# Optimization experiments

Hardware: AMD Instinct MI355X
Metric: run time of the kernel (lower is better)

The kernel has to match this reference:

```python
import jax, jax.numpy as jnp
import numpy as np
from jax import lax

# ---- static config (matches init_kwargs) ----
STRIDE = 16
BASE_SIZE = 16
SCALES = np.array([2., 4., 8., 16., 32.])
RATIOS = np.array([0.5, 1., 2.])
CLIP = 4.14
NMS_THRESH = 0.7
PRE_NMS = 6000
POST_NMS = 300
MIN_SIZE = 16.0


def _whctrs(a):
    w = a[2] - a[0] + 1.0
    h = a[3] - a[1] + 1.0
    return w, h, a[0] + 0.5 * (w - 1.0), a[1] + 0.5 * (h - 1.0)


def _mkanchors(ws, hs, xc, yc):
    return np.stack([xc - 0.5 * (ws - 1.0), yc - 0.5 * (hs - 1.0),
                     xc + 0.5 * (ws - 1.0), yc + 0.5 * (hs - 1.0)], axis=1)


def _base_anchors():
    ba = np.array([1.0, 1.0, BASE_SIZE, BASE_SIZE]) - 1.0
    w, h, xc, yc = _whctrs(ba)
    size = w * h
    ws = np.round(np.sqrt(size / RATIOS))
    hs = np.round(ws * RATIOS)
    ra = _mkanchors(ws, hs, xc, yc)
    out = []
    for i in range(ra.shape[0]):
        w, h, xc, yc = _whctrs(ra[i])
        out.append(_mkanchors(w * SCALES, h * SCALES, xc, yc))
    return np.concatenate(out, axis=0)  # (A,4), A = len(ratios)*len(scales)


def _grid_anchors(Hf, Wf):
    ba = _base_anchors()                       # (A,4)
    sx, sy = np.meshgrid(np.arange(Wf) * STRIDE, np.arange(Hf) * STRIDE)
    shifts = np.stack([sx, sy, sx, sy], axis=-1)          # (Hf,Wf,4)
    anch = shifts[:, :, None, :] + ba[None, None, :, :]    # (Hf,Wf,A,4)
    return jnp.asarray(anch.reshape(1, -1, 4), dtype=jnp.float32)


def _decode_clip(anchors, deltas, img_h, img_w):
    # NormalizedBoxCenterDecoder (stds=1) + clip to image
    aw = anchors[..., 2] - anchors[..., 0]
    ah = anchors[..., 3] - anchors[..., 1]
    ax = anchors[..., 0] + 0.5 * aw
    ay = anchors[..., 1] + 0.5 * ah
    dx, dy, dw, dh = deltas[..., 0], deltas[..., 1], deltas[..., 2], deltas[..., 3]
    ox = dx * aw + ax
    oy = dy * ah + ay
    ow = jnp.exp(jnp.minimum(dw, CLIP)) * aw * 0.5
    oh = jnp.exp(jnp.minimum(dh, CLIP)) * ah * 0.5
    x1 = jnp.clip(ox - ow, 0.0, img_w - 1.0)
    y1 = jnp.clip(oy - oh, 0.0, img_h - 1.0)
    x2 = jnp.clip(ox + ow, 0.0, img_w - 1.0)
    y2 = jnp.clip(oy + oh, 0.0, img_h - 1.0)
    return jnp.stack([x1, y1, x2, y2], axis=-1)


def _nms_single(scores, boxes):
    # scores (N,), boxes (N,4). Greedy NMS, force_suppress, sorted by score desc.
    order = jnp.argsort(-scores)[:PRE_NMS]
    s = scores[order]
    b = boxes[order]
    x1, y1, x2, y2 = b[:, 0], b[:, 1], b[:, 2], b[:, 3]
    area = (x2 - x1) * (y2 - y1)
    iw = jnp.maximum(jnp.minimum(x2[:, None], x2[None, :]) - jnp.maximum(x1[:, None], x1[None, :]), 0.0)
    ih = jnp.maximum(jnp.minimum(y2[:, None], y2[None, :]) - jnp.maximum(y1[:, None], y1[None, :]), 0.0)
    inter = iw * ih
    iou = inter / (area[:, None] + area[None, :] - inter + 1e-12)  # (PRE,PRE)

    supp0 = s < 0.0  # invalid entries (score set to -1 by min_size filter)

    def body(supp, i):
        keep = jnp.logical_not(supp[i])
        new = jnp.where(keep, jnp.logical_or(supp, iou[i] > NMS_THRESH), supp)
        new = new.at[i].set(supp[i])  # never self-suppress
        return new, None

    supp, _ = lax.scan(body, supp0, jnp.arange(PRE_NMS))
    kept = jnp.logical_not(supp)
    perm = jnp.argsort(jnp.where(kept, 0, 1), stable=True)  # kept boxes first, order preserved
    out_s = jnp.where(kept[perm], s[perm], -1.0)
    out_b = jnp.where(kept[perm][:, None], b[perm], -1.0)
    return out_s[:POST_NMS, None], out_b[:POST_NMS]


def _forward(img, x, conv_w, conv_b, score_w, score_b, loc_w, loc_b):
    B, _, Hf, Wf = x.shape
    img_h, img_w = float(img.shape[2]), float(img.shape[3])
    anchors = _grid_anchors(Hf, Wf)  # (1, Hf*Wf*A, 4)

    # conv1 3x3 pad 1 + ReLU
    h = lax.conv_general_dilated(x, conv_w, (1, 1), [(1, 1), (1, 1)],
                                 dimension_numbers=('NCHW', 'OIHW', 'NCHW'))
    h = jax.nn.relu(h + conv_b[None, :, None, None])

    A = score_w.shape[0]
    raw_scores = jnp.einsum('bchw,oc->bhwo', h, score_w.reshape(A, -1)) + score_b
    raw_scores = raw_scores.reshape(B, -1, 1)                       # (B,N,1)
    raw_boxes = jnp.einsum('bchw,oc->bhwo', h, loc_w.reshape(4 * A, -1)) + loc_b
    raw_boxes = raw_boxes.reshape(B, -1, 4)                         # (B,N,4)

    rpn_scores = jax.nn.sigmoid(raw_scores)

    roi = _decode_clip(anchors, raw_boxes, img_h, img_w)            # (B,N,4)
    width = roi[..., 2] - roi[..., 0]
    height = roi[..., 3] - roi[..., 1]
    invalid = jnp.logical_or(width < MIN_SIZE, height < MIN_SIZE)   # (B,N)
    score = jnp.where(invalid[..., None], -1.0, rpn_scores)         # (B,N,1)
    roi = jnp.where(invalid[..., None], -1.0, roi)

    out_s, out_b = jax.vmap(_nms_single)(score[..., 0], roi)        # (B,300,1),(B,300,4)
    return jnp.concatenate([out_s, out_b], axis=-1)                 # (B,300,5)


def setup_inputs() -> dict:
    key = jax.random.key(0)
    ks = jax.random.split(key, 8)
    img = jax.random.normal(ks[0], (1, 3, 1024, 1024), jnp.float32)
    x = jax.random.normal(ks[1], (1, 1024, 64, 64), jnp.float32)
    conv_w = jax.random.normal(ks[2], (1024, 1024, 3, 3), jnp.float32) * 0.01
    conv_b = jnp.zeros((1024,), jnp.float32)
    score_w = jax.random.normal(ks[3], (15, 1024, 1, 1), jnp.float32) * 0.01
    score_b = jnp.zeros((15,), jnp.float32)
    loc_w = jax.random.normal(ks[4], (60, 1024, 1, 1), jnp.float32) * 0.002
    loc_b = jnp.zeros((60,), jnp.float32)
    return {"img": img, "x": x, "conv_w": conv_w, "conv_b": conv_b,
            "score_w": score_w, "score_b": score_b, "loc_w": loc_w, "loc_b": loc_b}


def reference(img, x, conv_w, conv_b, score_w, score_b, loc_w, loc_b):
    return _forward(img, x, conv_w, conv_b, score_w, score_b, loc_w, loc_b)
```

## Files before the change

### kernel.cpp

```cpp
#include <hip/hip_runtime.h>

typedef unsigned int uint;
typedef unsigned short ushort;
typedef unsigned long long u64;

typedef __attribute__((ext_vector_type(8))) short short8;
typedef __attribute__((ext_vector_type(4))) float floatx4;

__device__ inline ushort bf16rne(float v) {
  uint b = __float_as_uint(v);
  uint r = (b + 0x7fffu + ((b >> 16) & 1u)) >> 16;
  return (ushort)r;
}

__device__ inline void gl_lds16(const void* g, void* l) {
  __builtin_amdgcn_global_load_lds(
      (const __attribute__((address_space(1))) unsigned int*)g,
      (__attribute__((address_space(3))) unsigned int*)l, 16, 0, 0);
}

__global__ __launch_bounds__(256) void prep_x(const float* __restrict__ x,
                                              ushort* __restrict__ xh,
                                              ushort* __restrict__ xl) {
  __shared__ float tile[64 * 65];
  int ci0 = blockIdx.x * 64, y = blockIdx.y, t = threadIdx.x;
#pragma unroll
  for (int it = 0; it < 16; ++it) {
    int L = t + 256 * it;
    int cl = L >> 6, xx = L & 63;
    tile[cl * 65 + xx] = x[(size_t)(ci0 + cl) * 4096 + y * 64 + xx];
  }
  __syncthreads();
#pragma unroll
  for (int it = 0; it < 16; ++it) {
    int L = t + 256 * it;
    int xx = L >> 6, cl = L & 63;
    float v = tile[cl * 65 + xx];
    ushort h2 = bf16rne(v);
    float hf = __uint_as_float((uint)h2 << 16);
    ushort l2 = bf16rne(v - hf);
    size_t oi = ((size_t)((y + 1) * 66 + (xx + 1))) * 1024 + ci0 + cl;
    xh[oi] = h2;
    xl[oi] = l2;
  }
}

__global__ __launch_bounds__(256) void prep_w(const float* __restrict__ w,
                                              ushort* __restrict__ wh,
                                              ushort* __restrict__ wl) {
  __shared__ float tile[2304];
  int co = blockIdx.x, ci0 = blockIdx.y * 256, t = threadIdx.x;
  const float* src = w + ((size_t)co * 1024 + ci0) * 9;
  for (int i = t; i < 2304; i += 256) tile[i] = src[i];
  __syncthreads();
  int ci = ci0 + t;
#pragma unroll
  for (int off = 0; off < 9; ++off) {
    float v = tile[t * 9 + off];
    ushort h2 = bf16rne(v);
    float hf = __uint_as_float((uint)h2 << 16);
    ushort l2 = bf16rne(v - hf);
    size_t oi = ((size_t)off << 20) | ((size_t)co << 10) | (size_t)ci;
    wh[oi] = h2;
    wl[oi] = l2;
  }
}

__global__ __launch_bounds__(256) void prep_head(
    const float* __restrict__ score_w, const float* __restrict__ loc_w,
    const float* __restrict__ score_b, const float* __restrict__ loc_b,
    ushort* __restrict__ wh, ushort* __restrict__ wl, float* __restrict__ bh) {
  int idx = blockIdx.x * 256 + threadIdx.x;
  int o = idx >> 10, ci = idx & 1023;
  float v = 0.f;
  if (o < 15) v = score_w[o * 1024 + ci];
  else if (o < 75) v = loc_w[(o - 15) * 1024 + ci];
  ushort h2 = bf16rne(v);
  float hf = __uint_as_float((uint)h2 << 16);
  wh[idx] = h2;
  wl[idx] = bf16rne(v - hf);
  if (idx < 128) bh[idx] = (idx < 15) ? score_b[idx] : ((idx < 75) ? loc_b[idx - 15] : 0.f);
}

template <int IM2COL>
__global__ __launch_bounds__(256, 1) void gemm_bf16x3(
    const ushort* __restrict__ Ahi, const ushort* __restrict__ Alo,
    const ushort* __restrict__ Bhi, const ushort* __restrict__ Blo,
    const float* __restrict__ bias, int nChunks, float* __restrict__ outRaw,
    ushort* __restrict__ outHi, ushort* __restrict__ outLo) {
  __shared__ ushort sm[2 * 4 * 128 * 32];
  const int t = threadIdx.x;
  const int m0 = blockIdx.x * 128;
  const int n0 = blockIdx.y * 128;

  auto stage = [&](int kc, int bufIdx) {
    char* lds = (char*)sm + bufIdx * 32768;
    int off = 0, cc = 0, oy = 0, ox = 0;
    if (IM2COL) {
      off = kc >> 5;
      cc = (kc & 31) << 5;
      oy = off / 3;
      ox = off - 3 * oy;
    }
#pragma unroll
    for (int q = 0; q < 2; ++q) {
      int L = t + 256 * q, row = L >> 2, seg = L & 3;
      size_t aoff, boff;
      if (IM2COL) {
        int m = m0 + row, y = m >> 6, xq = m & 63;
        aoff = ((size_t)((y + oy) * 66 + (xq + ox)) * 1024 + (size_t)cc) * 2 + seg * 16;
        boff = (((size_t)off << 20) + ((size_t)(n0 + row) << 10) + (size_t)cc) * 2 + seg * 16;
      } else {
        aoff = (((size_t)(m0 + row) << 10) + (size_t)kc * 32) * 2 + seg * 16;
        boff = (((size_t)(n0 + row) << 10) + (size_t)kc * 32) * 2 + seg * 16;
      }
      int dst = L * 16;
      gl_lds16((const char*)Ahi + aoff, lds + dst);
      gl_lds16((const char*)Alo + aoff, lds + 8192 + dst);
      gl_lds16((const char*)Bhi + boff, lds + 16384 + dst);
      gl_lds16((const char*)Blo + boff, lds + 24576 + dst);
    }
  };

  const int lane = t & 63, wv = t >> 6;
  const int wm = (wv & 1) * 64, wn = (wv >> 1) * 64;
  const int arow = wm + (lane & 15);
  const int brow = wn + (lane & 15);
  const int ko = (lane >> 4) * 8;

  floatx4 acc[4][4];
#pragma unroll
  for (int i = 0; i < 4; ++i)
#pragma unroll
    for (int j = 0; j < 4; ++j) acc[i][j] = (floatx4){0.f, 0.f, 0.f, 0.f};

  stage(0, 0);
  for (int kc = 0; kc < nChunks; ++kc) {
    __syncthreads();
    if (kc + 1 < nChunks) stage(kc + 1, (kc + 1) & 1);
    const ushort* sb = sm + (kc & 1) * 16384;
    const ushort* sAh = sb;
    const ushort* sAl = sb + 4096;
    const ushort* sBh = sb + 8192;
    const ushort* sBl = sb + 12288;
    short8 ah[4], al[4], bh2[4], bl2[4];
#pragma unroll
    for (int i = 0; i < 4; ++i) {
      ah[i] = *(const short8*)(sAh + (arow + 16 * i) * 32 + ko);
      al[i] = *(const short8*)(sAl + (arow + 16 * i) * 32 + ko);
      bh2[i] = *(const short8*)(sBh + (brow + 16 * i) * 32 + ko);
      bl2[i] = *(const short8*)(sBl + (brow + 16 * i) * 32 + ko);
    }
#pragma unroll
    for (int i = 0; i < 4; ++i)
#pragma unroll
      for (int j = 0; j < 4; ++j) {
        acc[i][j] = __builtin_amdgcn_mfma_f32_16x16x32_bf16(ah[i], bh2[j], acc[i][j], 0, 0, 0);
        acc[i][j] = __builtin_amdgcn_mfma_f32_16x16x32_bf16(ah[i], bl2[j], acc[i][j], 0, 0, 0);
        acc[i][j] = __builtin_amdgcn_mfma_f32_16x16x32_bf16(al[i], bh2[j], acc[i][j], 0, 0, 0);
      }
  }

#pragma unroll
  for (int i = 0; i < 4; ++i)
#pragma unroll
    for (int j = 0; j < 4; ++j) {
      int nn = n0 + wn + 16 * j + (lane & 15);
      float bv = bias[nn];
#pragma unroll
      for (int r = 0; r < 4; ++r) {
        int mm = m0 + wm + 16 * i + (lane >> 4) * 4 + r;
        float v = acc[i][j][r] + bv;
        if (IM2COL) {
          v = fmaxf(v, 0.f);
          ushort h2 = bf16rne(v);
          float hf = __uint_as_float((uint)h2 << 16);
          ushort l2 = bf16rne(v - hf);
          outHi[(size_t)mm * 1024 + nn] = h2;
          outLo[(size_t)mm * 1024 + nn] = l2;
        } else {
          outRaw[(size_t)mm * 128 + nn] = v;
        }
      }
    }
}

__global__ __launch_bounds__(256) void decode_k(const float* __restrict__ raw,
                                                float* __restrict__ scores,
                                                float4* __restrict__ boxes,
                                                uint* __restrict__ key32,
                                                uint* __restrict__ hist) {
  int i = blockIdx.x * 256 + threadIdx.x;
  int m = i / 15, a = i - m * 15;
  int y = m >> 6, x = m & 63;
  const float* rp = raw + (size_t)m * 128;
  float logit = rp[a];
  float dx = rp[15 + 4 * a], dy = rp[16 + 4 * a];
  float dw = rp[17 + 4 * a], dh = rp[18 + 4 * a];
  int rr = a / 5, ss = a - rr * 5;
  float sc5 = (float)(2 << ss);
  float W = ((rr == 0) ? 23.f : (rr == 1) ? 16.f : 11.f) * sc5;
  float H = ((rr == 0) ? 12.f : (rr == 1) ? 16.f : 22.f) * sc5;
  float aw = W - 1.f, ah = H - 1.f;
  float ax = x * 16.f + 7.5f, ay = y * 16.f + 7.5f;
  float ox = dx * aw + ax, oyc = dy * ah + ay;
  float ow = expf(fminf(dw, 4.14f)) * aw * 0.5f;
  float oh = expf(fminf(dh, 4.14f)) * ah * 0.5f;
  float x1 = fminf(fmaxf(ox - ow, 0.f), 1023.f);
  float y1 = fminf(fmaxf(oyc - oh, 0.f), 1023.f);
  float x2 = fminf(fmaxf(ox + ow, 0.f), 1023.f);
  float y2 = fminf(fmaxf(oyc + oh, 0.f), 1023.f);
  bool inval = ((x2 - x1) < 16.f) || ((y2 - y1) < 16.f);
  float sc = inval ? -1.f : (1.f / (1.f + expf(-logit)));
  scores[i] = sc;
  boxes[i] = inval ? make_float4(-1.f, -1.f, -1.f, -1.f) : make_float4(x1, y1, x2, y2);
  uint kb = __float_as_uint(sc);
  uint key = (kb & 0x80000000u) ? ~kb : (kb | 0x80000000u);
  key32[i] = key;
  atomicAdd(&hist[key >> 16], 1u);
}

__global__ __launch_bounds__(256) void find_t16(const uint* __restrict__ hist,
                                                uint* __restrict__ selT) {
  __shared__ uint ps[256];
  __shared__ int segS;
  int t = threadIdx.x;
  uint s = 0;
  const uint* hp = hist + t * 256;
  for (int i = 0; i < 256; ++i) s += hp[i];
  ps[t] = s;
  __syncthreads();
  for (int d = 1; d < 256; d <<= 1) {
    uint v = ps[t] + ((t + d < 256) ? ps[t + d] : 0u);
    __syncthreads();
    ps[t] = v;
    __syncthreads();
  }
  if (ps[t] >= 6000u && (t == 255 || ps[t + 1] < 6000u)) segS = t;
  __syncthreads();
  int sg = segS;
  uint base = (sg == 255) ? 0u : ps[sg + 1];
  uint h2 = hist[sg * 256 + t];
  __syncthreads();
  ps[t] = h2;
  __syncthreads();
  for (int d = 1; d < 256; d <<= 1) {
    uint v = ps[t] + ((t + d < 256) ? ps[t + d] : 0u);
    __syncthreads();
    ps[t] = v;
    __syncthreads();
  }
  if (base + ps[t] >= 6000u && (t == 255 || base + ps[t + 1] < 6000u))
    *selT = (uint)(sg * 256 + t);
}

__global__ __launch_bounds__(256) void gather_k(const uint* __restrict__ key32,
                                                const uint* __restrict__ selT,
                                                uint* __restrict__ cnt,
                                                u64* __restrict__ cand) {
  int i = blockIdx.x * 256 + threadIdx.x;
  uint T = *selT;
  uint k = key32[i];
  if ((k >> 16) >= T) {
    uint pos = atomicAdd(cnt, 1u);
    if (pos < 8192) cand[pos] = ((u64)k << 32) | (u64)(~(uint)i);
  }
}

__global__ __launch_bounds__(1024) void sort_gather(
    const u64* __restrict__ cand, const uint* __restrict__ cnt,
    const float* __restrict__ scores, const float4* __restrict__ boxes,
    float* __restrict__ sortedS, float4* __restrict__ sortedB) {
  extern __shared__ u64 sk[];
  int t = threadIdx.x;
  int C = (int)*cnt;
  if (C > 8192) C = 8192;
  for (int j = t; j < 8192; j += 1024) sk[j] = (j < C) ? cand[j] : 0ull;
  __syncthreads();
  for (int k = 2; k <= 8192; k <<= 1) {
    for (int j2 = k >> 1; j2 > 0; j2 >>= 1) {
      for (int p = t; p < 4096; p += 1024) {
        int i = ((p & ~(j2 - 1)) << 1) | (p & (j2 - 1));
        int ix = i | j2;
        u64 a = sk[i], b = sk[ix];
        bool ddir = (i & k) != 0;
        if ((a < b) != ddir) { sk[i] = b; sk[ix] = a; }
      }
      __syncthreads();
    }
  }
  for (int j = t; j < 6016; j += 1024) {
    if (j < 6000) {
      u64 key = sk[j];
      uint idx = ~(uint)(key & 0xffffffffu);
      sortedS[j] = scores[idx];
      sortedB[j] = boxes[idx];
    } else {
      sortedS[j] = -1.f;
      sortedB[j] = make_float4(0.f, 0.f, 0.f, 0.f);
    }
  }
}

__global__ __launch_bounds__(64) void iou_mask(const float4* __restrict__ boxes,
                                               u64* __restrict__ mask) {
  __shared__ float cx1[64], cy1[64], cx2[64], cy2[64], car[64];
  int bi = blockIdx.x, bj = blockIdx.y, t = threadIdx.x;
  float4 cb = boxes[bj * 64 + t];
  cx1[t] = cb.x; cy1[t] = cb.y; cx2[t] = cb.z; cy2[t] = cb.w;
  car[t] = (cb.z - cb.x) * (cb.w - cb.y);
  __syncthreads();
  int r = bi * 64 + t;
  float4 rb = boxes[r];
  float ra = (rb.z - rb.x) * (rb.w - rb.y);
  u64 wd = 0;
#pragma unroll 8
  for (int j = 0; j < 64; ++j) {
    float iw = fmaxf(fminf(rb.z, cx2[j]) - fmaxf(rb.x, cx1[j]), 0.f);
    float ih = fmaxf(fminf(rb.w, cy2[j]) - fmaxf(rb.y, cy1[j]), 0.f);
    float inter = iw * ih;
    float iou = inter / (ra + car[j] - inter + 1e-12f);
    if (iou > 0.7f && r != bj * 64 + j) wd |= (1ull << j);
  }
  mask[(size_t)r * 128 + bj] = wd;
}

__global__ __launch_bounds__(64) void nms_scan(const u64* __restrict__ mask,
                                               const float* __restrict__ sortedS,
                                               const float4* __restrict__ sortedB,
                                               float* __restrict__ out) {
  __shared__ int klist[300];
  int lane = threadIdx.x;
  u64 Sx = 0, Sy = 0;
  for (int w2 = 0; w2 < 94; ++w2) {
    bool neg = sortedS[w2 * 64 + lane] < 0.f;
    u64 m2 = __ballot(neg);
    if ((w2 >> 1) == lane) { if (w2 & 1) Sy = m2; else Sx = m2; }
  }
  int count = 0;
  for (int w2 = 0; w2 < 94; ++w2) {
    u64 cur = __shfl((w2 & 1) ? Sy : Sx, w2 >> 1);
    u64 rem = ~cur;
    if (w2 == 93) rem &= (1ull << 48) - 1;
    while (rem) {
      int b = __builtin_ctzll(rem);
      int i = w2 * 64 + b;
      if (lane == 0) klist[count] = i;
      count++;
      if (count == 300) goto done;
      const ulonglong2* rp = (const ulonglong2*)(mask + (size_t)i * 128);
      ulonglong2 rv = rp[lane];
      Sx |= rv.x;
      Sy |= rv.y;
      u64 cur2 = __shfl((w2 & 1) ? Sy : Sx, w2 >> 1);
      rem &= ~cur2;
      rem &= (b == 63) ? 0ull : (~0ull << (b + 1));
    }
  }
done:
  __syncthreads();
  for (int j = lane; j < 300; j += 64) {
    float s;
    float4 bb;
    if (j < count) {
      int i = klist[j];
      s = sortedS[i];
      bb = sortedB[i];
    } else {
      s = -1.f;
      bb = make_float4(-1.f, -1.f, -1.f, -1.f);
    }
    out[j * 5 + 0] = s;
    out[j * 5 + 1] = bb.x;
    out[j * 5 + 2] = bb.y;
    out[j * 5 + 3] = bb.z;
    out[j * 5 + 4] = bb.w;
  }
}

constexpr size_t O_XH = 0;
constexpr size_t O_XL = 8921088;
constexpr size_t O_WTH = 17842176;
constexpr size_t O_WTL = 36716544;
constexpr size_t O_HH = 55590912;
constexpr size_t O_HL = 63979520;
constexpr size_t O_WHH = 72368128;
constexpr size_t O_WHL = 72630272;
constexpr size_t O_BHD = 72892416;
constexpr size_t O_SC = 72892928;
constexpr size_t O_BX = 73138688;
constexpr size_t O_KEY = 74121728;
constexpr size_t O_HIST = 74367488;
constexpr size_t O_CNT = 74629632;
constexpr size_t O_CAND = 74629888;
constexpr size_t O_SELT = 74695424;
constexpr size_t O_SS = 74695680;
constexpr size_t O_SB = 74719744;
constexpr size_t O_RAW = 0;
constexpr size_t O_MASK = 17842176;

extern "C" void kernel_launch(void* const* d_in, const int* in_sizes, int n_in,
                              void* d_out, int out_size, void* d_ws,
                              size_t ws_size, hipStream_t stream) {
  (void)in_sizes; (void)n_in; (void)out_size; (void)ws_size;
  const float* x = (const float*)d_in[1];
  const float* conv_w = (const float*)d_in[2];
  const float* conv_b = (const float*)d_in[3];
  const float* score_w = (const float*)d_in[4];
  const float* score_b = (const float*)d_in[5];
  const float* loc_w = (const float*)d_in[6];
  const float* loc_b = (const float*)d_in[7];
  float* out = (float*)d_out;
  char* ws = (char*)d_ws;

  ushort* xh = (ushort*)(ws + O_XH);
  ushort* xl = (ushort*)(ws + O_XL);
  ushort* wTh = (ushort*)(ws + O_WTH);
  ushort* wTl = (ushort*)(ws + O_WTL);
  ushort* hh = (ushort*)(ws + O_HH);
  ushort* hl = (ushort*)(ws + O_HL);
  ushort* wHh = (ushort*)(ws + O_WHH);
  ushort* wHl = (ushort*)(ws + O_WHL);
  float* biasH = (float*)(ws + O_BHD);
  float* raw = (float*)(ws + O_RAW);
  float* scores = (float*)(ws + O_SC);
  float4* boxes = (float4*)(ws + O_BX);
  uint* key32 = (uint*)(ws + O_KEY);
  uint* hist = (uint*)(ws + O_HIST);
  uint* cnt = (uint*)(ws + O_CNT);
  u64* cand = (u64*)(ws + O_CAND);
  uint* selT = (uint*)(ws + O_SELT);
  float* sortedS = (float*)(ws + O_SS);
  float4* sortedB = (float4*)(ws + O_SB);
  u64* mask = (u64*)(ws + O_MASK);

  hipMemsetAsync(ws + O_XH, 0, 2 * 8921088, stream);
  hipMemsetAsync(ws + O_HIST, 0, 262144 + 256, stream);

  prep_x<<<dim3(16, 64), 256, 0, stream>>>(x, xh, xl);
  prep_w<<<dim3(1024, 4), 256, 0, stream>>>(conv_w, wTh, wTl);
  prep_head<<<512, 256, 0, stream>>>(score_w, loc_w, score_b, loc_b, wHh, wHl, biasH);

  gemm_bf16x3<1><<<dim3(32, 8), 256, 0, stream>>>(xh, xl, wTh, wTl, conv_b, 288,
                                                  nullptr, hh, hl);
  gemm_bf16x3<0><<<dim3(32, 1), 256, 0, stream>>>(hh, hl, wHh, wHl, biasH, 32,
                                                  raw, nullptr, nullptr);

  decode_k<<<240, 256, 0, stream>>>(raw, scores, boxes, key32, hist);
  find_t16<<<1, 256, 0, stream>>>(hist, selT);
  gather_k<<<240, 256, 0, stream>>>(key32, selT, cnt, cand);
  sort_gather<<<1, 1024, 65536, stream>>>(cand, cnt, scores, boxes, sortedS, sortedB);
  iou_mask<<<dim3(94, 94), 64, 0, stream>>>(sortedB, mask);
  nms_scan<<<1, 64, 0, stream>>>(mask, sortedS, sortedB, out);
}
```

Before: 743.9 us.

## Replace single-block bitonic sort with histogram bucket scatter and per-bucket sorts

Replaces the single-workgroup 8192-element bitonic sort of the top-k candidates with an exclusive scan over the 65536-bin score histogram. Candidates are scattered directly into their bucket positions, then each small bucket is sorted in parallel by its own workgroup. The NMS scan also prefetches the next candidate's mask row so its load overlaps the current iteration. This removes a long serial-ish sort in one block but adds extra kernel launches, a memset, and atomics per bucket.

```diff
diff --git a/kernel.cpp b/kernel.cpp
--- a/kernel.cpp
+++ b/kernel.cpp
@@ -220,85 +220,100 @@
   atomicAdd(&hist[key >> 16], 1u);
 }
 
-__global__ __launch_bounds__(256) void find_t16(const uint* __restrict__ hist,
-                                                uint* __restrict__ selT) {
-  __shared__ uint ps[256];
-  __shared__ int segS;
+__global__ __launch_bounds__(1024) void scan_hist(const uint* __restrict__ hist,
+                                                  uint* __restrict__ bbase,
+                                                  uint* __restrict__ selC) {
+  __shared__ uint cs[1024];
   int t = threadIdx.x;
+  const uint* hp = hist + t * 64;
   uint s = 0;
-  const uint* hp = hist + t * 256;
-  for (int i = 0; i < 256; ++i) s += hp[i];
-  ps[t] = s;
+#pragma unroll 8
+  for (int i = 0; i < 64; ++i) s += hp[i];
+  cs[t] = s;
   __syncthreads();
-  for (int d = 1; d < 256; d <<= 1) {
-    uint v = ps[t] + ((t + d < 256) ? ps[t + d] : 0u);
+  for (int d = 1; d < 1024; d <<= 1) {
+    uint v = cs[t] + ((t + d < 1024) ? cs[t + d] : 0u);
     __syncthreads();
-    ps[t] = v;
+    cs[t] = v;
     __syncthreads();
   }
-  if (ps[t] >= 6000u && (t == 255 || ps[t + 1] < 6000u)) segS = t;
-  __syncthreads();
-  int sg = segS;
-  uint base = (sg == 255) ? 0u : ps[sg + 1];
-  uint h2 = hist[sg * 256 + t];
-  __syncthreads();
-  ps[t] = h2;
-  __syncthreads();
-  for (int d = 1; d < 256; d <<= 1) {
-    uint v = ps[t] + ((t + d < 256) ? ps[t + d] : 0u);
+  uint above = (t < 1023) ? cs[t + 1] : 0u;
+  uint run = 0;
+  for (int i = 63; i >= 0; --i) {
+    uint h = hp[i];
+    uint ca = above + run;
+    bbase[t * 64 + i] = ca;
+    if (ca < 6000u && ca + h >= 6000u) {
+      selC[0] = (uint)(t * 64 + i);
+      selC[1] = ca + h;
+    }
+    run += h;
+  }
+}
+
+__global__ __launch_bounds__(256) void scatter_k(const uint* __restrict__ key32,
+                                                 const uint* __restrict__ bbase,
+                                                 const uint* __restrict__ selC,
+                                                 uint* __restrict__ fill,
+                                                 u64* __restrict__ sby) {
+  int i = blockIdx.x * 256 + threadIdx.x;
+  uint k = key32[i];
+  uint b = k >> 16;
+  if (b >= selC[0]) {
+    uint pos = bbase[b] + atomicAdd(&fill[b], 1u);
+    if (pos < 8192) sby[pos] = ((u64)k << 32) | (u64)(~(uint)i);
+  }
+}
+
+__global__ __launch_bounds__(64) void bucket_sort(const uint* __restrict__ bbase,
+                                                  const uint* __restrict__ selC,
+                                                  u64* __restrict__ sby) {
+  __shared__ u64 sk[4096];
+  uint T = selC[0], C = selC[1];
+  int lane = threadIdx.x;
+  for (uint b = T + blockIdx.x; b < 65536u; b += 8192u) {
+    uint base = bbase[b];
+    if (base >= 6000u) continue;
+    uint incl = (b == 0) ? C : bbase[b - 1];
+    uint n = incl - base;
+    if (n < 2u || n > 4096u) continue;
+    if (base + n > 8192u) continue;
+    uint np2 = 1;
+    while (np2 < n) np2 <<= 1;
+    for (uint j = lane; j < np2; j += 64) sk[j] = (j < n) ? sby[base + j] : 0ull;
     __syncthreads();
-    ps[t] = v;
+    for (uint k = 2; k <= np2; k <<= 1) {
+      for (uint j2 = k >> 1; j2 > 0; j2 >>= 1) {
+        for (uint p = lane; p < (np2 >> 1); p += 64) {
+          uint i1 = ((p & ~(j2 - 1)) << 1) | (p & (j2 - 1));
+          uint ix = i1 | j2;
+          u64 a = sk[i1], c = sk[ix];
+          bool descseg = (i1 & k) == 0;
+          if ((a < c) == descseg) { sk[i1] = c; sk[ix] = a; }
+        }
+        __syncthreads();
+      }
+    }
+    for (uint j = lane; j < n; j += 64) sby[base + j] = sk[j];
     __syncthreads();
   }
-  if (base + ps[t] >= 6000u && (t == 255 || base + ps[t + 1] < 6000u))
-    *selT = (uint)(sg * 256 + t);
-}
-
-__global__ __launch_bounds__(256) void gather_k(const uint* __restrict__ key32,
-                                                const uint* __restrict__ selT,
-                                                uint* __restrict__ cnt,
-                                                u64* __restrict__ cand) {
-  int i = blockIdx.x * 256 + threadIdx.x;
-  uint T = *selT;
-  uint k = key32[i];
-  if ((k >> 16) >= T) {
-    uint pos = atomicAdd(cnt, 1u);
-    if (pos < 8192) cand[pos] = ((u64)k << 32) | (u64)(~(uint)i);
-  }
-}
-
-__global__ __launch_bounds__(1024) void sort_gather(
-    const u64* __restrict__ cand, const uint* __restrict__ cnt,
-    const float* __restrict__ scores, const float4* __restrict__ boxes,
-    float* __restrict__ sortedS, float4* __restrict__ sortedB) {
-  extern __shared__ u64 sk[];
-  int t = threadIdx.x;
-  int C = (int)*cnt;
-  if (C > 8192) C = 8192;
-  for (int j = t; j < 8192; j += 1024) sk[j] = (j < C) ? cand[j] : 0ull;
-  __syncthreads();
-  for (int k = 2; k <= 8192; k <<= 1) {
-    for (int j2 = k >> 1; j2 > 0; j2 >>= 1) {
-      for (int p = t; p < 4096; p += 1024) {
-        int i = ((p & ~(j2 - 1)) << 1) | (p & (j2 - 1));
-        int ix = i | j2;
-        u64 a = sk[i], b = sk[ix];
-        bool ddir = (i & k) != 0;
-        if ((a < b) != ddir) { sk[i] = b; sk[ix] = a; }
-      }
-      __syncthreads();
-    }
-  }
-  for (int j = t; j < 6016; j += 1024) {
-    if (j < 6000) {
-      u64 key = sk[j];
-      uint idx = ~(uint)(key & 0xffffffffu);
-      sortedS[j] = scores[idx];
-      sortedB[j] = boxes[idx];
-    } else {
-      sortedS[j] = -1.f;
-      sortedB[j] = make_float4(0.f, 0.f, 0.f, 0.f);
-    }
+}
+
+__global__ __launch_bounds__(256) void gather_sorted(
+    const u64* __restrict__ sby, const float* __restrict__ scores,
+    const float4* __restrict__ boxes, float* __restrict__ sortedS,
+    float4* __restrict__ sortedB) {
+  int j = blockIdx.x * 256 + threadIdx.x;
+  if (j >= 6016) return;
+  if (j < 6000) {
+    u64 key = sby[j];
+    uint idx = ~(uint)(key & 0xffffffffu);
+    if (idx >= 61440u) idx = 61439u;
+    sortedS[j] = scores[idx];
+    sortedB[j] = boxes[idx];
+  } else {
+    sortedS[j] = -1.f;
+    sortedB[j] = make_float4(0.f, 0.f, 0.f, 0.f);
   }
 }
 
@@ -329,7 +344,7 @@
                                                const float* __restrict__ sortedS,
                                                const float4* __restrict__ sortedB,
                                                float* __restrict__ out) {
-  __shared__ int klist[300];
+  __shared__ int klist[304];
   int lane = threadIdx.x;
   u64 Sx = 0, Sy = 0;
   for (int w2 = 0; w2 < 94; ++w2) {
@@ -338,26 +353,35 @@
     if ((w2 >> 1) == lane) { if (w2 & 1) Sy = m2; else Sx = m2; }
   }
   int count = 0;
-  for (int w2 = 0; w2 < 94; ++w2) {
+  for (int w2 = 0; w2 < 94 && count < 300; ++w2) {
     u64 cur = __shfl((w2 & 1) ? Sy : Sx, w2 >> 1);
     u64 rem = ~cur;
     if (w2 == 93) rem &= (1ull << 48) - 1;
+    int pf_i = -1;
+    ulonglong2 pf;
     while (rem) {
       int b = __builtin_ctzll(rem);
       int i = w2 * 64 + b;
+      u64 rem2 = (b == 63) ? 0ull : (rem & (~0ull << (b + 1)));
+      ulonglong2 rv;
+      if (i == pf_i) rv = pf;
+      else rv = ((const ulonglong2*)(mask + (size_t)i * 128))[lane];
+      if (rem2) {
+        int nb = __builtin_ctzll(rem2);
+        pf_i = w2 * 64 + nb;
+        pf = ((const ulonglong2*)(mask + (size_t)pf_i * 128))[lane];
+      } else {
+        pf_i = -1;
+      }
       if (lane == 0) klist[count] = i;
       count++;
-      if (count == 300) goto done;
-      const ulonglong2* rp = (const ulonglong2*)(mask + (size_t)i * 128);
-      ulonglong2 rv = rp[lane];
+      if (count == 300) break;
       Sx |= rv.x;
       Sy |= rv.y;
       u64 cur2 = __shfl((w2 & 1) ? Sy : Sx, w2 >> 1);
-      rem &= ~cur2;
-      rem &= (b == 63) ? 0ull : (~0ull << (b + 1));
-    }
-  }
-done:
+      rem = rem2 & ~cur2;
+    }
+  }
   __syncthreads();
   for (int j = lane; j < 300; j += 64) {
     float s;
@@ -391,11 +415,11 @@
 constexpr size_t O_BX = 73138688;
 constexpr size_t O_KEY = 74121728;
 constexpr size_t O_HIST = 74367488;
-constexpr size_t O_CNT = 74629632;
-constexpr size_t O_CAND = 74629888;
-constexpr size_t O_SELT = 74695424;
-constexpr size_t O_SS = 74695680;
-constexpr size_t O_SB = 74719744;
+constexpr size_t O_BBASE = 74629632;
+constexpr size_t O_SELC = 74891776;
+constexpr size_t O_SBY = 74892032;
+constexpr size_t O_SS = 74957568;
+constexpr size_t O_SB = 74981632;
 constexpr size_t O_RAW = 0;
 constexpr size_t O_MASK = 17842176;
 
@@ -427,15 +451,15 @@
   float4* boxes = (float4*)(ws + O_BX);
   uint* key32 = (uint*)(ws + O_KEY);
   uint* hist = (uint*)(ws + O_HIST);
-  uint* cnt = (uint*)(ws + O_CNT);
-  u64* cand = (u64*)(ws + O_CAND);
-  uint* selT = (uint*)(ws + O_SELT);
+  uint* bbase = (uint*)(ws + O_BBASE);
+  uint* selC = (uint*)(ws + O_SELC);
+  u64* sby = (u64*)(ws + O_SBY);
   float* sortedS = (float*)(ws + O_SS);
   float4* sortedB = (float4*)(ws + O_SB);
   u64* mask = (u64*)(ws + O_MASK);
 
   hipMemsetAsync(ws + O_XH, 0, 2 * 8921088, stream);
-  hipMemsetAsync(ws + O_HIST, 0, 262144 + 256, stream);
+  hipMemsetAsync(ws + O_HIST, 0, 262144, stream);
 
   prep_x<<<dim3(16, 64), 256, 0, stream>>>(x, xh, xl);
   prep_w<<<dim3(1024, 4), 256, 0, stream>>>(conv_w, wTh, wTl);
@@ -447,9 +471,11 @@
                                                   raw, nullptr, nullptr);
 
   decode_k<<<240, 256, 0, stream>>>(raw, scores, boxes, key32, hist);
-  find_t16<<<1, 256, 0, stream>>>(hist, selT);
-  gather_k<<<240, 256, 0, stream>>>(key32, selT, cnt, cand);
-  sort_gather<<<1, 1024, 65536, stream>>>(cand, cnt, scores, boxes, sortedS, sortedB);
+  scan_hist<<<1, 1024, 0, stream>>>(hist, bbase, selC);
+  hipMemsetAsync(ws + O_HIST, 0, 262144, stream);
+  scatter_k<<<240, 256, 0, stream>>>(key32, bbase, selC, hist, sby);
+  bucket_sort<<<8192, 64, 0, stream>>>(bbase, selC, sby);
+  gather_sorted<<<24, 256, 0, stream>>>(sby, scores, boxes, sortedS, sortedB);
   iou_mask<<<dim3(94, 94), 64, 0, stream>>>(sortedB, mask);
   nms_scan<<<1, 64, 0, stream>>>(mask, sortedS, sortedB, out);
 }
```

New measurement: 820.4 us. 10.3% more time.
